# Performance work log

Measured on AMD Instinct MI355X. Metric: run time of the kernel, lower is better.

Reference implementation:

```python
import jax, jax.numpy as jnp
import numpy as np

N = 50000
E = 800000
F = 64
HID = 64
HEADS = 4
NTYPES = 3


def layer_norm(x, g, b, eps=1e-5):
    mu = x.mean(-1, keepdims=True)
    var = ((x - mu) ** 2).mean(-1, keepdims=True)
    return (x - mu) * jax.lax.rsqrt(var + eps) * g + b


def gat_conv(x, src, dst, n, W, att_src, att_dst, bias, concat):
    # PyG GATConv: per-head linear transform, additive attention, segment softmax over dst.
    H, C = att_src.shape
    xp = (x @ W).reshape(n, H, C)                       # [N,H,C]
    a_s = (xp * att_src).sum(-1)                         # [N,H]
    a_d = (xp * att_dst).sum(-1)                         # [N,H]
    e = jax.nn.leaky_relu(a_s[src] + a_d[dst], 0.2)      # [Etot,H]
    m = jax.ops.segment_max(e, dst, num_segments=n)      # stable softmax per target
    ex = jnp.exp(e - m[dst])
    denom = jax.ops.segment_sum(ex, dst, num_segments=n)
    alpha = ex / (denom[dst] + 1e-16)                    # [Etot,H]
    msg = xp[src] * alpha[:, :, None]                    # [Etot,H,C]
    out = jax.ops.segment_sum(msg, dst, num_segments=n)  # [N,H,C]
    out = out.reshape(n, H * C) if concat else out.mean(1)
    return out + bias


def setup_inputs() -> dict:
    key = jax.random.key(0)
    ks = jax.random.split(key, 12)
    f32 = jnp.float32
    return {
        'node_features': jax.random.normal(ks[0], (N, F), f32),
        'node_types': jax.random.randint(ks[1], (N,), 0, NTYPES),
        'edge_index': jax.random.randint(ks[2], (2, E), 0, N),
        'type_emb': jax.random.normal(ks[3], (NTYPES, HID), f32) * 0.02,
        'proj_W': jax.random.normal(ks[4], (F, HID), f32) / np.sqrt(F).astype(np.float32),
        'proj_b': jnp.zeros((HID,), f32),
        'W0': jax.random.normal(ks[5], (HID, HEADS * HID), f32) / np.sqrt(HID).astype(np.float32),
        'att_src0': jax.random.normal(ks[6], (HEADS, HID), f32) * 0.1,
        'att_dst0': jax.random.normal(ks[7], (HEADS, HID), f32) * 0.1,
        'bias0': jnp.zeros((HEADS * HID,), f32),
        'ln0_g': jnp.ones((HEADS * HID,), f32),
        'ln0_b': jnp.zeros((HEADS * HID,), f32),
        'W1': jax.random.normal(ks[8], (HEADS * HID, HEADS * HID), f32) / np.sqrt(HEADS * HID).astype(np.float32),
        'att_src1': jax.random.normal(ks[9], (HEADS, HID), f32) * 0.1,
        'att_dst1': jax.random.normal(ks[10], (HEADS, HID), f32) * 0.1,
        'bias1': jnp.zeros((HID,), f32),
        'ln1_g': jnp.ones((HID,), f32),
        'ln1_b': jnp.zeros((HID,), f32),
    }


def reference(node_features, node_types, edge_index, type_emb, proj_W, proj_b,
              W0, att_src0, att_dst0, bias0, ln0_g, ln0_b,
              W1, att_src1, att_dst1, bias1, ln1_g, ln1_b):
    n = node_features.shape[0]
    loop = jnp.arange(n)
    src = jnp.concatenate([edge_index[0], loop])  # add_self_loops=True (PyG default)
    dst = jnp.concatenate([edge_index[1], loop])
    # input projection + node-type embedding
    x = node_features @ proj_W + proj_b + type_emb[node_types]
    # layer 0: concat heads -> [N, HEADS*HID]
    h = gat_conv(x, src, dst, n, W0, att_src0, att_dst0, bias0, True)
    h = jax.nn.relu(layer_norm(h, ln0_g, ln0_b))  # dropout is identity in eval
    # layer 1: mean over heads -> [N, HID]; residual skipped (shape mismatch 256 vs 64)
    h2 = gat_conv(h, src, dst, n, W1, att_src1, att_dst1, bias1, False)
    h2 = jax.nn.relu(layer_norm(h2, ln1_g, ln1_b))
    return h2
```

## Files before the change

### kernel.cpp

```cpp
#include <hip/hip_runtime.h>
#include <hip/hip_bf16.h>
#include <hip/hip_fp16.h>

typedef unsigned short u16;
typedef unsigned int u32;
typedef short s16x8 __attribute__((ext_vector_type(8)));
typedef float f32x4 __attribute__((ext_vector_type(4)));

__device__ __forceinline__ float bf2f(u16 u) {
  return __uint_as_float(((u32)u) << 16);
}

__device__ __forceinline__ u16 f2b(float f) {
  __hip_bfloat16 h = __float2bfloat16(f);
  return *(u16*)&h;
}

__device__ __forceinline__ u32 packbf(float lo, float hi) {
  return (u32)f2b(lo) | ((u32)f2b(hi) << 16);
}

__device__ __forceinline__ bool sniff_bf16(const void* ones) {
  u32 w = *(const u32*)ones;
  return (w >> 16) == (w & 0xFFFFu);
}

__device__ __forceinline__ float ldf(const void* p, size_t i, bool bf) {
  return bf ? bf2f(((const u16*)p)[i]) : ((const float*)p)[i];
}

__device__ __forceinline__ float rdlane_f(float v, int e) {
  return __uint_as_float((u32)__builtin_amdgcn_readlane((int)__float_as_uint(v), e));
}

__global__ void fill_f32(float* __restrict__ p, float v, size_t n) {
  size_t i = (size_t)blockIdx.x * blockDim.x + threadIdx.x;
  if (i < n) p[i] = v;
}

__global__ __launch_bounds__(256) void deg_count_k(const int* __restrict__ ei, int E, int N,
                                                   int* __restrict__ deg) {
  int i = blockIdx.x * 256 + threadIdx.x;
  if (i >= E + N) return;
  int d = (i < E) ? ei[E + i] : (i - E);
  atomicAdd(deg + d, 1);
}

__global__ __launch_bounds__(256) void scan_local_k(const int* __restrict__ deg,
                                                    int* __restrict__ off,
                                                    int* __restrict__ bsum, int N) {
  __shared__ int ps[256];
  int t = threadIdx.x;
  int i = blockIdx.x * 256 + t;
  int v = (i < N) ? deg[i] : 0;
  ps[t] = v;
  __syncthreads();
#pragma unroll
  for (int o = 1; o < 256; o <<= 1) {
    int u = (t >= o) ? ps[t - o] : 0;
    __syncthreads();
    ps[t] += u;
    __syncthreads();
  }
  if (i < N) off[i] = ps[t] - v;
  if (t == 255) bsum[blockIdx.x] = ps[255];
}

__global__ __launch_bounds__(1024) void scan_bsum_k(int* __restrict__ bsum, int nb) {
  __shared__ int ps[1024];
  int t = threadIdx.x;
  int v = (t < nb) ? bsum[t] : 0;
  ps[t] = v;
  __syncthreads();
#pragma unroll
  for (int o = 1; o < 1024; o <<= 1) {
    int u = (t >= o) ? ps[t - o] : 0;
    __syncthreads();
    ps[t] += u;
    __syncthreads();
  }
  if (t < nb) bsum[t] = ps[t] - v;
}

__global__ __launch_bounds__(256) void scan_add_k(int* __restrict__ off,
                                                  const int* __restrict__ bsum,
                                                  int* __restrict__ cur, int N, int Etot) {
  int i = blockIdx.x * 256 + threadIdx.x;
  if (i == 0) off[N] = Etot;
  if (i >= N) return;
  int o = off[i] + bsum[i >> 8];
  off[i] = o;
  cur[i] = o;
}

__global__ __launch_bounds__(256) void scatter_k(const int* __restrict__ ei, int E, int N,
                                                 int* __restrict__ cur, int* __restrict__ csr) {
  int i = blockIdx.x * 256 + threadIdx.x;
  if (i >= E + N) return;
  int s, d;
  if (i < E) { s = ei[i]; d = ei[E + i]; } else { s = i - E; d = s; }
  int p = atomicAdd(cur + d, 1);
  csr[p] = s;
}

__global__ __launch_bounds__(256) void wpack_k(const void* __restrict__ W,
                                               const void* __restrict__ ones,
                                               u16* __restrict__ Wp, int K) {
  bool bf = sniff_bf16(ones);
  int i = blockIdx.x * 256 + threadIdx.x;
  if (i >= K * 256) return;
  int j = i & 7;
  int q = (i >> 3) & 3;
  int c = (i >> 5) & 255;
  int kc = i >> 13;
  int k = kc * 32 + q * 8 + j;
  Wp[i] = f2b(ldf(W, (size_t)k * 256 + c, bf));
}

__global__ __launch_bounds__(256) void wpack64_k(const void* __restrict__ W,
                                                 const void* __restrict__ ones,
                                                 u16* __restrict__ Wp) {
  bool bf = sniff_bf16(ones);
  int i = blockIdx.x * 256 + threadIdx.x;
  if (i >= 64 * 64) return;
  int j = i & 7;
  int q = (i >> 3) & 3;
  int c = (i >> 5) & 63;
  int kc = i >> 11;
  int k = kc * 32 + q * 8 + j;
  Wp[i] = f2b(ldf(W, (size_t)k * 64 + c, bf));
}

__global__ __launch_bounds__(256) void l0_gemm_k(
    const void* __restrict__ nf, const int* __restrict__ ntype,
    const u16* __restrict__ Wpp, const void* __restrict__ pbias,
    const void* __restrict__ temb, const u16* __restrict__ Wp,
    const void* __restrict__ atts, const void* __restrict__ attd,
    const void* __restrict__ ones,
    u16* __restrict__ C, float* __restrict__ aS, float* __restrict__ aD, int N) {
  bool bf = sniff_bf16(ones);
  __shared__ u16 xs[16][64];
  int t = threadIdx.x;
  int wave = t >> 6, lane = t & 63;
  int r = lane & 15, q = lane >> 4;
  int row0 = blockIdx.x * 16;
  int arow = row0 + r;
  if (arow >= N) arow = N - 1;
  f32x4 xacc = {0.f, 0.f, 0.f, 0.f};
#pragma unroll
  for (int kc = 0; kc < 2; kc++) {
    s16x8 a;
    if (bf) {
      a = *(const s16x8*)((const u16*)nf + (size_t)arow * 64 + kc * 32 + q * 8);
    } else {
      const float* fp = (const float*)nf + (size_t)arow * 64 + kc * 32 + q * 8;
#pragma unroll
      for (int j = 0; j < 8; j++) a[j] = (short)f2b(fp[j]);
    }
    int c = wave * 16 + r;
    s16x8 b = *(const s16x8*)(Wpp + (((size_t)kc * 64 + c) * 4 + q) * 8);
    xacc = __builtin_amdgcn_mfma_f32_16x16x32_bf16(a, b, xacc, 0, 0, 0);
  }
#pragma unroll
  for (int rg = 0; rg < 4; rg++) {
    int row = row0 + q * 4 + rg;
    int rl = (row < N) ? row : N - 1;
    int col = wave * 16 + r;
    int ty = ntype[rl];
    float v = xacc[rg] + ldf(pbias, col, bf) + ldf(temb, ty * 64 + col, bf);
    xs[q * 4 + rg][col] = f2b(v);
  }
  __syncthreads();
  int colw = wave * 64;
  f32x4 acc[4] = {{0.f, 0.f, 0.f, 0.f}, {0.f, 0.f, 0.f, 0.f},
                  {0.f, 0.f, 0.f, 0.f}, {0.f, 0.f, 0.f, 0.f}};
#pragma unroll
  for (int kc = 0; kc < 2; kc++) {
    s16x8 a = *(const s16x8*)&xs[r][kc * 32 + q * 8];
#pragma unroll
    for (int ct = 0; ct < 4; ct++) {
      int c = colw + ct * 16 + r;
      s16x8 b = *(const s16x8*)(Wp + (((size_t)kc * 256 + c) * 4 + q) * 8);
      acc[ct] = __builtin_amdgcn_mfma_f32_16x16x32_bf16(a, b, acc[ct], 0, 0, 0);
    }
  }
#pragma unroll
  for (int ct = 0; ct < 4; ct++) {
#pragma unroll
    for (int rg = 0; rg < 4; rg++) {
      int row = row0 + q * 4 + rg;
      if (row < N) C[(size_t)row * 256 + colw + ct * 16 + r] = f2b(acc[ct][rg]);
    }
  }
  float sp[4] = {0.f, 0.f, 0.f, 0.f};
  float dp[4] = {0.f, 0.f, 0.f, 0.f};
#pragma unroll
  for (int ct = 0; ct < 4; ct++) {
    int c = colw + ct * 16 + r;
    float av = ldf(atts, c, bf);
    float dv = ldf(attd, c, bf);
#pragma unroll
    for (int rg = 0; rg < 4; rg++) {
      sp[rg] += acc[ct][rg] * av;
      dp[rg] += acc[ct][rg] * dv;
    }
  }
#pragma unroll
  for (int o = 1; o < 16; o <<= 1) {
#pragma unroll
    for (int rg = 0; rg < 4; rg++) {
      sp[rg] += __shfl_xor(sp[rg], o, 64);
      dp[rg] += __shfl_xor(dp[rg], o, 64);
    }
  }
  if (r == 0) {
#pragma unroll
    for (int rg = 0; rg < 4; rg++) {
      int row = row0 + q * 4 + rg;
      if (row < N) {
        aS[(size_t)row * 4 + wave] = sp[rg];
        aD[(size_t)row * 4 + wave] = dp[rg];
      }
    }
  }
}

template <int K>
__global__ __launch_bounds__(256) void gemm_mfma_k(
    const u16* __restrict__ A, const u16* __restrict__ Wp,
    const void* __restrict__ atts, const void* __restrict__ attd,
    const void* __restrict__ ones,
    u16* __restrict__ C, float* __restrict__ aS, float* __restrict__ aD, int N) {
  bool bf = sniff_bf16(ones);
  int t = threadIdx.x;
  int wave = t >> 6, lane = t & 63;
  int r = lane & 15, q = lane >> 4;
  int row0 = blockIdx.x * 16;
  int colw = wave * 64;
  int arow = row0 + r;
  if (arow >= N) arow = N - 1;
  const u16* ap = A + (size_t)arow * K + q * 8;
  f32x4 acc[4] = {{0.f, 0.f, 0.f, 0.f}, {0.f, 0.f, 0.f, 0.f},
                  {0.f, 0.f, 0.f, 0.f}, {0.f, 0.f, 0.f, 0.f}};
#pragma unroll
  for (int kc = 0; kc < K / 32; kc++) {
    s16x8 a = *(const s16x8*)(ap + kc * 32);
#pragma unroll
    for (int ct = 0; ct < 4; ct++) {
      int c = colw + ct * 16 + r;
      s16x8 b = *(const s16x8*)(Wp + (((size_t)kc * 256 + c) * 4 + q) * 8);
      acc[ct] = __builtin_amdgcn_mfma_f32_16x16x32_bf16(a, b, acc[ct], 0, 0, 0);
    }
  }
#pragma unroll
  for (int ct = 0; ct < 4; ct++) {
#pragma unroll
    for (int rg = 0; rg < 4; rg++) {
      int row = row0 + q * 4 + rg;
      if (row < N) C[(size_t)row * 256 + colw + ct * 16 + r] = f2b(acc[ct][rg]);
    }
  }
  float sp[4] = {0.f, 0.f, 0.f, 0.f};
  float dp[4] = {0.f, 0.f, 0.f, 0.f};
#pragma unroll
  for (int ct = 0; ct < 4; ct++) {
    int c = colw + ct * 16 + r;
    float av = ldf(atts, c, bf);
    float dv = ldf(attd, c, bf);
#pragma unroll
    for (int rg = 0; rg < 4; rg++) {
      sp[rg] += acc[ct][rg] * av;
      dp[rg] += acc[ct][rg] * dv;
    }
  }
#pragma unroll
  for (int o = 1; o < 16; o <<= 1) {
#pragma unroll
    for (int rg = 0; rg < 4; rg++) {
      sp[rg] += __shfl_xor(sp[rg], o, 64);
      dp[rg] += __shfl_xor(dp[rg], o, 64);
    }
  }
  if (r == 0) {
#pragma unroll
    for (int rg = 0; rg < 4; rg++) {
      int row = row0 + q * 4 + rg;
      if (row < N) {
        aS[(size_t)row * 4 + wave] = sp[rg];
        aD[(size_t)row * 4 + wave] = dp[rg];
      }
    }
  }
}

template <int LAYER>
__global__ __launch_bounds__(256) void agg_fused_k(
    const int* __restrict__ off, const int* __restrict__ csr,
    const float* __restrict__ aS, const float* __restrict__ aD,
    const u16* __restrict__ xp,
    const void* __restrict__ bias, const void* __restrict__ g,
    const void* __restrict__ b, void* __restrict__ out, int N) {
  bool bf = sniff_bf16(g);
  int n = blockIdx.x * 4 + (threadIdx.x >> 6);
  int lane = threadIdx.x & 63;
  if (n >= N) return;
  int start = off[n], end = off[n + 1];
  bool hiSel = (lane & 32) != 0;
  float4 ad4 = *(const float4*)(aD + (size_t)n * 4);
  float ad[4] = {ad4.x, ad4.y, ad4.z, ad4.w};
  float den[4] = {0.f, 0.f, 0.f, 0.f};
  float acc[4] = {0.f, 0.f, 0.f, 0.f};
  const u32* xp32 = (const u32*)xp;

  for (int cs = start; cs < end; cs += 64) {
    int cnt = end - cs; if (cnt > 64) cnt = 64;
    int s = 0;
    float ex[4] = {0.f, 0.f, 0.f, 0.f};
    if (lane < cnt) {
      s = csr[cs + lane];
      float4 as4 = *(const float4*)(aS + (size_t)s * 4);
      float av[4] = {as4.x, as4.y, as4.z, as4.w};
#pragma unroll
      for (int h = 0; h < 4; h++) {
        float v = av[h] + ad[h];
        v = (v > 0.f ? v : 0.2f * v) - 3.0f;
        ex[h] = __expf(v);
        den[h] += ex[h];
      }
    }
#pragma unroll 4
    for (int e = 0; e < cnt; e++) {
      int se = __builtin_amdgcn_readlane(s, e);
      float w0 = rdlane_f(ex[0], e);
      float w1 = rdlane_f(ex[1], e);
      float w2 = rdlane_f(ex[2], e);
      float w3 = rdlane_f(ex[3], e);
      float wA = hiSel ? w1 : w0;
      float wB = hiSel ? w3 : w2;
      const u32* xr = xp32 + (size_t)se * 128 + lane;
      u32 dA = xr[0];
      u32 dB = xr[64];
      acc[0] += wA * __uint_as_float(dA << 16);
      acc[1] += wA * __uint_as_float(dA & 0xffff0000u);
      acc[2] += wB * __uint_as_float(dB << 16);
      acc[3] += wB * __uint_as_float(dB & 0xffff0000u);
    }
  }
#pragma unroll
  for (int h = 0; h < 4; h++) {
#pragma unroll
    for (int o = 32; o > 0; o >>= 1) den[h] += __shfl_xor(den[h], o, 64);
  }
  {
    float dA = (hiSel ? den[1] : den[0]) + 1e-16f;
    float dB = (hiSel ? den[3] : den[2]) + 1e-16f;
    acc[0] /= dA; acc[1] /= dA;
    acc[2] /= dB; acc[3] /= dB;
  }

  if (LAYER == 0) {
    int c0 = 2 * lane, c2 = 128 + 2 * lane;
    float y[4];
    y[0] = acc[0] + ldf(bias, c0, bf);
    y[1] = acc[1] + ldf(bias, c0 + 1, bf);
    y[2] = acc[2] + ldf(bias, c2, bf);
    y[3] = acc[3] + ldf(bias, c2 + 1, bf);
    float sum = y[0] + y[1] + y[2] + y[3];
#pragma unroll
    for (int o = 32; o > 0; o >>= 1) sum += __shfl_xor(sum, o, 64);
    float mu = sum * (1.f / 256.f);
    float sq = 0.f;
#pragma unroll
    for (int j = 0; j < 4; j++) { float dv = y[j] - mu; sq += dv * dv; }
#pragma unroll
    for (int o = 32; o > 0; o >>= 1) sq += __shfl_xor(sq, o, 64);
    float inv = rsqrtf(sq * (1.f / 256.f) + 1e-5f);
    float o0 = fmaxf((y[0] - mu) * inv * ldf(g, c0, bf) + ldf(b, c0, bf), 0.f);
    float o1 = fmaxf((y[1] - mu) * inv * ldf(g, c0 + 1, bf) + ldf(b, c0 + 1, bf), 0.f);
    float o2 = fmaxf((y[2] - mu) * inv * ldf(g, c2, bf) + ldf(b, c2, bf), 0.f);
    float o3 = fmaxf((y[3] - mu) * inv * ldf(g, c2 + 1, bf) + ldf(b, c2 + 1, bf), 0.f);
    u32* orow = (u32*)out + (size_t)n * 128;
    orow[lane] = packbf(o0, o1);
    orow[64 + lane] = packbf(o2, o3);
  } else {
    float p0 = acc[0] + acc[2];
    float p1 = acc[1] + acc[3];
    p0 += __shfl_xor(p0, 32, 64);
    p1 += __shfl_xor(p1, 32, 64);
    int c = 2 * (lane & 31);
    float z0 = 0.25f * p0 + ldf(bias, c, bf);
    float z1 = 0.25f * p1 + ldf(bias, c + 1, bf);
    float sum = z0 + z1;
#pragma unroll
    for (int o = 32; o > 0; o >>= 1) sum += __shfl_xor(sum, o, 64);
    float mu = sum * (1.f / 128.f);
    float d0 = z0 - mu, d1 = z1 - mu;
    float sq = d0 * d0 + d1 * d1;
#pragma unroll
    for (int o = 32; o > 0; o >>= 1) sq += __shfl_xor(sq, o, 64);
    float inv = rsqrtf(sq * (1.f / 128.f) + 1e-5f);
    float y0 = fmaxf(d0 * inv * ldf(g, c, bf) + ldf(b, c, bf), 0.f);
    float y1 = fmaxf(d1 * inv * ldf(g, c + 1, bf) + ldf(b, c + 1, bf), 0.f);
    if (lane < 32) {
      if (bf) {
        ((u32*)out)[(size_t)n * 32 + lane] = packbf(y0, y1);
      } else {
        ((float2*)out)[(size_t)n * 32 + lane] = make_float2(y0, y1);
      }
    }
  }
}

extern "C" void kernel_launch(void* const* d_in, const int* in_sizes, int n_in,
                              void* d_out, int out_size, void* d_ws, size_t ws_size,
                              hipStream_t stream) {
  const void* nf   = d_in[0];
  const int* ntyp  = (const int*)d_in[1];
  const int* ei    = (const int*)d_in[2];
  const void* temb = d_in[3];
  const void* pW   = d_in[4];
  const void* pb   = d_in[5];
  const void* W0   = d_in[6];
  const void* as0  = d_in[7];
  const void* ad0  = d_in[8];
  const void* b0   = d_in[9];
  const void* g0   = d_in[10];
  const void* be0  = d_in[11];
  const void* W1   = d_in[12];
  const void* as1  = d_in[13];
  const void* ad1  = d_in[14];
  const void* b1   = d_in[15];
  const void* g1   = d_in[16];
  const void* be1  = d_in[17];

  int N = in_sizes[0] / 64;
  int E = in_sizes[2] / 2;
  int Etot = E + N;

  u16* Wp0 = (u16*)d_ws;
  u16* Wp1 = Wp0 + 64 * 256;
  u16* Wpp = Wp1 + 256 * 256;
  u16* A   = Wpp + 64 * 64;
  u16* hb  = A + (size_t)N * 256;
  float* aS = (float*)(hb + (size_t)N * 256);
  float* aD = aS + (size_t)N * 4;
  int* deg  = (int*)(aD + (size_t)N * 4);
  int* off  = deg + N;
  int* csr  = off + N + 1;
  int* bsum = csr + Etot;

  dim3 b256(256);
  int nodeBlocks = (N + 3) / 4;
  int edgeBlocksT = (Etot + 255) / 256;
  int gemmBlocks = (N + 15) / 16;
  int scanBlocks = (N + 255) / 256;

  fill_f32<<<(N + 255) / 256, b256, 0, stream>>>((float*)deg, 0.f, (size_t)N);
  deg_count_k<<<edgeBlocksT, b256, 0, stream>>>(ei, E, N, deg);
  scan_local_k<<<scanBlocks, b256, 0, stream>>>(deg, off, bsum, N);
  scan_bsum_k<<<1, 1024, 0, stream>>>(bsum, scanBlocks);
  scan_add_k<<<scanBlocks, b256, 0, stream>>>(off, bsum, deg, N, Etot);
  scatter_k<<<edgeBlocksT, b256, 0, stream>>>(ei, E, N, deg, csr);
  wpack_k<<<(64 * 256 + 255) / 256, b256, 0, stream>>>(W0, g0, Wp0, 64);
  wpack_k<<<(256 * 256 + 255) / 256, b256, 0, stream>>>(W1, g0, Wp1, 256);
  wpack64_k<<<(64 * 64 + 255) / 256, b256, 0, stream>>>(pW, g0, Wpp);

  l0_gemm_k<<<gemmBlocks, b256, 0, stream>>>(nf, ntyp, Wpp, pb, temb, Wp0, as0, ad0, g0,
                                             A, aS, aD, N);
  agg_fused_k<0><<<nodeBlocks, b256, 0, stream>>>(off, csr, aS, aD, A, b0, g0, be0, hb, N);

  gemm_mfma_k<256><<<gemmBlocks, b256, 0, stream>>>(hb, Wp1, as1, ad1, g0, A, aS, aD, N);
  agg_fused_k<1><<<nodeBlocks, b256, 0, stream>>>(off, csr, aS, aD, A, b1, g1, be1, d_out, N);
}
```

Baseline: 417.8 us.

## Aggregate 64-dim projected features before W0 in layer 0, folding attention into vectors

Layer 0 is reordered using linearity. Edges now gather and softmax-weight the 64-wide projected features per head, and the W0 GEMM plus bias, LayerNorm and ReLU run after aggregation in a new post kernel. The attention logits come from precomputed vectors W0·att_src and W0·att_dst, so the [N,256] transformed features are no longer needed before aggregation. This cuts per-edge gather bytes by about four times. In exchange it adds an extra kernel and an N×256 intermediate written and read back, and bf16 rounding now happens at different points.

```diff
diff --git a/kernel.cpp b/kernel.cpp
--- a/kernel.cpp
+++ b/kernel.cpp
@@ -131,13 +131,30 @@
   Wp[i] = f2b(ldf(W, (size_t)k * 64 + c, bf));
 }
 
-__global__ __launch_bounds__(256) void l0_gemm_k(
+__global__ __launch_bounds__(256) void attvec_k(const void* __restrict__ W,
+                                                const void* __restrict__ atts,
+                                                const void* __restrict__ attd,
+                                                const void* __restrict__ ones,
+                                                float* __restrict__ va, float* __restrict__ vd) {
+  bool bf = sniff_bf16(ones);
+  int t = threadIdx.x;
+  int h = t >> 6, k = t & 63;
+  float s = 0.f, d = 0.f;
+  for (int c = 0; c < 64; c++) {
+    float w = ldf(W, (size_t)k * 256 + h * 64 + c, bf);
+    s += w * ldf(atts, h * 64 + c, bf);
+    d += w * ldf(attd, h * 64 + c, bf);
+  }
+  va[t] = s;
+  vd[t] = d;
+}
+
+__global__ __launch_bounds__(256) void proj_k(
     const void* __restrict__ nf, const int* __restrict__ ntype,
     const u16* __restrict__ Wpp, const void* __restrict__ pbias,
-    const void* __restrict__ temb, const u16* __restrict__ Wp,
-    const void* __restrict__ atts, const void* __restrict__ attd,
-    const void* __restrict__ ones,
-    u16* __restrict__ C, float* __restrict__ aS, float* __restrict__ aD, int N) {
+    const void* __restrict__ temb, const float* __restrict__ va,
+    const float* __restrict__ vd, const void* __restrict__ ones,
+    u16* __restrict__ x, float* __restrict__ aS, float* __restrict__ aD, int N) {
   bool bf = sniff_bf16(ones);
   __shared__ u16 xs[16][64];
   int t = threadIdx.x;
@@ -168,58 +185,162 @@
     int col = wave * 16 + r;
     int ty = ntype[rl];
     float v = xacc[rg] + ldf(pbias, col, bf) + ldf(temb, ty * 64 + col, bf);
-    xs[q * 4 + rg][col] = f2b(v);
+    u16 xb = f2b(v);
+    xs[q * 4 + rg][col] = xb;
+    if (row < N) x[(size_t)row * 64 + col] = xb;
   }
   __syncthreads();
-  int colw = wave * 64;
+  float vs[4], vdl[4];
+#pragma unroll
+  for (int h = 0; h < 4; h++) { vs[h] = va[h * 64 + lane]; vdl[h] = vd[h * 64 + lane]; }
+#pragma unroll
+  for (int rr = 0; rr < 4; rr++) {
+    int row = row0 + wave * 4 + rr;
+    float xv = bf2f(xs[wave * 4 + rr][lane]);
+    float ps[4], pd[4];
+#pragma unroll
+    for (int h = 0; h < 4; h++) { ps[h] = xv * vs[h]; pd[h] = xv * vdl[h]; }
+#pragma unroll
+    for (int o = 32; o > 0; o >>= 1) {
+#pragma unroll
+      for (int h = 0; h < 4; h++) {
+        ps[h] += __shfl_xor(ps[h], o, 64);
+        pd[h] += __shfl_xor(pd[h], o, 64);
+      }
+    }
+    if (lane == 0 && row < N) {
+#pragma unroll
+      for (int h = 0; h < 4; h++) {
+        aS[(size_t)row * 4 + h] = ps[h];
+        aD[(size_t)row * 4 + h] = pd[h];
+      }
+    }
+  }
+}
+
+__global__ __launch_bounds__(256) void agg0_k(
+    const int* __restrict__ off, const int* __restrict__ csr,
+    const float* __restrict__ aS, const float* __restrict__ aD,
+    const u16* __restrict__ x, u16* __restrict__ Ag, int N) {
+  int n = blockIdx.x * 4 + (threadIdx.x >> 6);
+  int lane = threadIdx.x & 63;
+  if (n >= N) return;
+  int start = off[n], end = off[n + 1];
+  float4 ad4 = *(const float4*)(aD + (size_t)n * 4);
+  float ad[4] = {ad4.x, ad4.y, ad4.z, ad4.w};
+  float den[4] = {0.f, 0.f, 0.f, 0.f};
+  float acc[4] = {0.f, 0.f, 0.f, 0.f};
+  const u16* xl = x + lane;
+
+  for (int cs = start; cs < end; cs += 64) {
+    int cnt = end - cs; if (cnt > 64) cnt = 64;
+    int s = 0;
+    float ex[4] = {0.f, 0.f, 0.f, 0.f};
+    if (lane < cnt) {
+      s = csr[cs + lane];
+      float4 as4 = *(const float4*)(aS + (size_t)s * 4);
+      float av[4] = {as4.x, as4.y, as4.z, as4.w};
+#pragma unroll
+      for (int h = 0; h < 4; h++) {
+        float v = av[h] + ad[h];
+        v = (v > 0.f ? v : 0.2f * v) - 3.0f;
+        ex[h] = __expf(v);
+        den[h] += ex[h];
+      }
+    }
+#pragma unroll 4
+    for (int e = 0; e < cnt; e++) {
+      int se = __builtin_amdgcn_readlane(s, e);
+      float w0 = rdlane_f(ex[0], e);
+      float w1 = rdlane_f(ex[1], e);
+      float w2 = rdlane_f(ex[2], e);
+      float w3 = rdlane_f(ex[3], e);
+      float xv = bf2f(xl[(size_t)se * 64]);
+      acc[0] += w0 * xv;
+      acc[1] += w1 * xv;
+      acc[2] += w2 * xv;
+      acc[3] += w3 * xv;
+    }
+  }
+#pragma unroll
+  for (int h = 0; h < 4; h++) {
+#pragma unroll
+    for (int o = 32; o > 0; o >>= 1) den[h] += __shfl_xor(den[h], o, 64);
+    acc[h] /= (den[h] + 1e-16f);
+  }
+#pragma unroll
+  for (int h = 0; h < 4; h++) Ag[(size_t)n * 256 + h * 64 + lane] = f2b(acc[h]);
+}
+
+__global__ __launch_bounds__(256) void l0post_k(
+    const u16* __restrict__ Ag, const u16* __restrict__ Wp,
+    const void* __restrict__ bias, const void* __restrict__ g,
+    const void* __restrict__ b, const void* __restrict__ ones,
+    u16* __restrict__ hb, int N) {
+  bool bf = sniff_bf16(ones);
+  __shared__ float sm_s[4][16], sm_q[4][16];
+  int t = threadIdx.x;
+  int wave = t >> 6, lane = t & 63;
+  int r = lane & 15, q = lane >> 4;
+  int row0 = blockIdx.x * 16;
+  int arow = row0 + r;
+  if (arow >= N) arow = N - 1;
+  const u16* ap = Ag + (size_t)arow * 256 + wave * 64 + q * 8;
   f32x4 acc[4] = {{0.f, 0.f, 0.f, 0.f}, {0.f, 0.f, 0.f, 0.f},
                   {0.f, 0.f, 0.f, 0.f}, {0.f, 0.f, 0.f, 0.f}};
 #pragma unroll
   for (int kc = 0; kc < 2; kc++) {
-    s16x8 a = *(const s16x8*)&xs[r][kc * 32 + q * 8];
+    s16x8 a = *(const s16x8*)(ap + kc * 32);
 #pragma unroll
     for (int ct = 0; ct < 4; ct++) {
-      int c = colw + ct * 16 + r;
-      s16x8 b = *(const s16x8*)(Wp + (((size_t)kc * 256 + c) * 4 + q) * 8);
-      acc[ct] = __builtin_amdgcn_mfma_f32_16x16x32_bf16(a, b, acc[ct], 0, 0, 0);
-    }
-  }
+      int c = wave * 64 + ct * 16 + r;
+      s16x8 bb = *(const s16x8*)(Wp + (((size_t)kc * 256 + c) * 4 + q) * 8);
+      acc[ct] = __builtin_amdgcn_mfma_f32_16x16x32_bf16(a, bb, acc[ct], 0, 0, 0);
+    }
+  }
+  float yv[4][4];
+  float s_p[4] = {0.f, 0.f, 0.f, 0.f};
+  float q_p[4] = {0.f, 0.f, 0.f, 0.f};
 #pragma unroll
   for (int ct = 0; ct < 4; ct++) {
-#pragma unroll
-    for (int rg = 0; rg < 4; rg++) {
-      int row = row0 + q * 4 + rg;
-      if (row < N) C[(size_t)row * 256 + colw + ct * 16 + r] = f2b(acc[ct][rg]);
-    }
-  }
-  float sp[4] = {0.f, 0.f, 0.f, 0.f};
-  float dp[4] = {0.f, 0.f, 0.f, 0.f};
-#pragma unroll
-  for (int ct = 0; ct < 4; ct++) {
-    int c = colw + ct * 16 + r;
-    float av = ldf(atts, c, bf);
-    float dv = ldf(attd, c, bf);
-#pragma unroll
-    for (int rg = 0; rg < 4; rg++) {
-      sp[rg] += acc[ct][rg] * av;
-      dp[rg] += acc[ct][rg] * dv;
+    float bc = ldf(bias, wave * 64 + ct * 16 + r, bf);
+#pragma unroll
+    for (int rg = 0; rg < 4; rg++) {
+      float y = acc[ct][rg] + bc;
+      yv[ct][rg] = y;
+      s_p[rg] += y;
+      q_p[rg] += y * y;
     }
   }
 #pragma unroll
   for (int o = 1; o < 16; o <<= 1) {
 #pragma unroll
     for (int rg = 0; rg < 4; rg++) {
-      sp[rg] += __shfl_xor(sp[rg], o, 64);
-      dp[rg] += __shfl_xor(dp[rg], o, 64);
+      s_p[rg] += __shfl_xor(s_p[rg], o, 64);
+      q_p[rg] += __shfl_xor(q_p[rg], o, 64);
     }
   }
   if (r == 0) {
 #pragma unroll
     for (int rg = 0; rg < 4; rg++) {
-      int row = row0 + q * 4 + rg;
-      if (row < N) {
-        aS[(size_t)row * 4 + wave] = sp[rg];
-        aD[(size_t)row * 4 + wave] = dp[rg];
+      sm_s[wave][q * 4 + rg] = s_p[rg];
+      sm_q[wave][q * 4 + rg] = q_p[rg];
+    }
+  }
+  __syncthreads();
+#pragma unroll
+  for (int rg = 0; rg < 4; rg++) {
+    int lr = q * 4 + rg;
+    int row = row0 + lr;
+    float mu = (sm_s[0][lr] + sm_s[1][lr] + sm_s[2][lr] + sm_s[3][lr]) * (1.f / 256.f);
+    float vq = (sm_q[0][lr] + sm_q[1][lr] + sm_q[2][lr] + sm_q[3][lr]) * (1.f / 256.f) - mu * mu;
+    float inv = rsqrtf(vq + 1e-5f);
+    if (row < N) {
+#pragma unroll
+      for (int ct = 0; ct < 4; ct++) {
+        int c = wave * 64 + ct * 16 + r;
+        float o_ = (yv[ct][rg] - mu) * inv * ldf(g, c, bf) + ldf(b, c, bf);
+        hb[(size_t)row * 256 + c] = f2b(fmaxf(o_, 0.f));
       }
     }
   }
@@ -293,8 +414,7 @@
   }
 }
 
-template <int LAYER>
-__global__ __launch_bounds__(256) void agg_fused_k(
+__global__ __launch_bounds__(256) void agg1_k(
     const int* __restrict__ off, const int* __restrict__ csr,
     const float* __restrict__ aS, const float* __restrict__ aD,
     const u16* __restrict__ xp,
@@ -357,56 +477,29 @@
     acc[0] /= dA; acc[1] /= dA;
     acc[2] /= dB; acc[3] /= dB;
   }
-
-  if (LAYER == 0) {
-    int c0 = 2 * lane, c2 = 128 + 2 * lane;
-    float y[4];
-    y[0] = acc[0] + ldf(bias, c0, bf);
-    y[1] = acc[1] + ldf(bias, c0 + 1, bf);
-    y[2] = acc[2] + ldf(bias, c2, bf);
-    y[3] = acc[3] + ldf(bias, c2 + 1, bf);
-    float sum = y[0] + y[1] + y[2] + y[3];
-#pragma unroll
-    for (int o = 32; o > 0; o >>= 1) sum += __shfl_xor(sum, o, 64);
-    float mu = sum * (1.f / 256.f);
-    float sq = 0.f;
-#pragma unroll
-    for (int j = 0; j < 4; j++) { float dv = y[j] - mu; sq += dv * dv; }
-#pragma unroll
-    for (int o = 32; o > 0; o >>= 1) sq += __shfl_xor(sq, o, 64);
-    float inv = rsqrtf(sq * (1.f / 256.f) + 1e-5f);
-    float o0 = fmaxf((y[0] - mu) * inv * ldf(g, c0, bf) + ldf(b, c0, bf), 0.f);
-    float o1 = fmaxf((y[1] - mu) * inv * ldf(g, c0 + 1, bf) + ldf(b, c0 + 1, bf), 0.f);
-    float o2 = fmaxf((y[2] - mu) * inv * ldf(g, c2, bf) + ldf(b, c2, bf), 0.f);
-    float o3 = fmaxf((y[3] - mu) * inv * ldf(g, c2 + 1, bf) + ldf(b, c2 + 1, bf), 0.f);
-    u32* orow = (u32*)out + (size_t)n * 128;
-    orow[lane] = packbf(o0, o1);
-    orow[64 + lane] = packbf(o2, o3);
-  } else {
-    float p0 = acc[0] + acc[2];
-    float p1 = acc[1] + acc[3];
-    p0 += __shfl_xor(p0, 32, 64);
-    p1 += __shfl_xor(p1, 32, 64);
-    int c = 2 * (lane & 31);
-    float z0 = 0.25f * p0 + ldf(bias, c, bf);
-    float z1 = 0.25f * p1 + ldf(bias, c + 1, bf);
-    float sum = z0 + z1;
-#pragma unroll
-    for (int o = 32; o > 0; o >>= 1) sum += __shfl_xor(sum, o, 64);
-    float mu = sum * (1.f / 128.f);
-    float d0 = z0 - mu, d1 = z1 - mu;
-    float sq = d0 * d0 + d1 * d1;
-#pragma unroll
-    for (int o = 32; o > 0; o >>= 1) sq += __shfl_xor(sq, o, 64);
-    float inv = rsqrtf(sq * (1.f / 128.f) + 1e-5f);
-    float y0 = fmaxf(d0 * inv * ldf(g, c, bf) + ldf(b, c, bf), 0.f);
-    float y1 = fmaxf(d1 * inv * ldf(g, c + 1, bf) + ldf(b, c + 1, bf), 0.f);
-    if (lane < 32) {
-      if (bf) {
-        ((u32*)out)[(size_t)n * 32 + lane] = packbf(y0, y1);
-      } else {
-        ((float2*)out)[(size_t)n * 32 + lane] = make_float2(y0, y1);
-      }
+  float p0 = acc[0] + acc[2];
+  float p1 = acc[1] + acc[3];
+  p0 += __shfl_xor(p0, 32, 64);
+  p1 += __shfl_xor(p1, 32, 64);
+  int c = 2 * (lane & 31);
+  float z0 = 0.25f * p0 + ldf(bias, c, bf);
+  float z1 = 0.25f * p1 + ldf(bias, c + 1, bf);
+  float sum = z0 + z1;
+#pragma unroll
+  for (int o = 32; o > 0; o >>= 1) sum += __shfl_xor(sum, o, 64);
+  float mu = sum * (1.f / 128.f);
+  float d0 = z0 - mu, d1 = z1 - mu;
+  float sq = d0 * d0 + d1 * d1;
+#pragma unroll
+  for (int o = 32; o > 0; o >>= 1) sq += __shfl_xor(sq, o, 64);
+  float inv = rsqrtf(sq * (1.f / 128.f) + 1e-5f);
+  float y0 = fmaxf(d0 * inv * ldf(g, c, bf) + ldf(b, c, bf), 0.f);
+  float y1 = fmaxf(d1 * inv * ldf(g, c + 1, bf) + ldf(b, c + 1, bf), 0.f);
+  if (lane < 32) {
+    if (bf) {
+      ((u32*)out)[(size_t)n * 32 + lane] = packbf(y0, y1);
+    } else {
+      ((float2*)out)[(size_t)n * 32 + lane] = make_float2(y0, y1);
     }
   }
 }
@@ -440,9 +533,13 @@
   u16* Wp0 = (u16*)d_ws;
   u16* Wp1 = Wp0 + 64 * 256;
   u16* Wpp = Wp1 + 256 * 256;
-  u16* A   = Wpp + 64 * 64;
+  u16* xb  = Wpp + 64 * 64;
+  u16* Ag  = xb + (size_t)N * 64;
+  u16* A   = Ag + (size_t)N * 256;
   u16* hb  = A + (size_t)N * 256;
-  float* aS = (float*)(hb + (size_t)N * 256);
+  float* va = (float*)(hb + (size_t)N * 256);
+  float* vd = va + 256;
+  float* aS = vd + 256;
   float* aD = aS + (size_t)N * 4;
   int* deg  = (int*)(aD + (size_t)N * 4);
   int* off  = deg + N;
@@ -464,11 +561,13 @@
   wpack_k<<<(64 * 256 + 255) / 256, b256, 0, stream>>>(W0, g0, Wp0, 64);
   wpack_k<<<(256 * 256 + 255) / 256, b256, 0, stream>>>(W1, g0, Wp1, 256);
   wpack64_k<<<(64 * 64 + 255) / 256, b256, 0, stream>>>(pW, g0, Wpp);
-
-  l0_gemm_k<<<gemmBlocks, b256, 0, stream>>>(nf, ntyp, Wpp, pb, temb, Wp0, as0, ad0, g0,
-                                             A, aS, aD, N);
-  agg_fused_k<0><<<nodeBlocks, b256, 0, stream>>>(off, csr, aS, aD, A, b0, g0, be0, hb, N);
+  attvec_k<<<1, b256, 0, stream>>>(W0, as0, ad0, g0, va, vd);
+
+  proj_k<<<gemmBlocks, b256, 0, stream>>>(nf, ntyp, Wpp, pb, temb, va, vd, g0,
+                                          xb, aS, aD, N);
+  agg0_k<<<nodeBlocks, b256, 0, stream>>>(off, csr, aS, aD, xb, Ag, N);
+  l0post_k<<<gemmBlocks, b256, 0, stream>>>(Ag, Wp0, b0, g0, be0, g0, hb, N);
 
   gemm_mfma_k<256><<<gemmBlocks, b256, 0, stream>>>(hb, Wp1, as1, ad1, g0, A, aS, aD, N);
-  agg_fused_k<1><<<nodeBlocks, b256, 0, stream>>>(off, csr, aS, aD, A, b1, g1, be1, d_out, N);
-}
+  agg1_k<<<nodeBlocks, b256, 0, stream>>>(off, csr, aS, aD, A, b1, g1, be1, d_out, N);
+}
```

Result: slower. 447.7 us (+7.1%).
